# Performance work log

Measured on AMD Instinct MI355X. Metric: run time of the kernel, lower is better.

Reference implementation:

```python
import jax, jax.numpy as jnp
import numpy as np

# SmallViT config (reconstructed; see shape_source)
B, C, H, W = 1024, 3, 32, 32
P = 4                # patch size
D = 128              # embed dim
NH, DH = 4, 32       # heads, head dim
FF = 256             # mlp hidden
L = 4                # encoder layers
T = (H // P) * (W // P) + 1  # 65 tokens
NQ = 4               # qubits
EPS = 1e-5


def layer_norm(x, s, b):
    m = x.mean(-1, keepdims=True)
    v = ((x - m) ** 2).mean(-1, keepdims=True)
    return (x - m) * jax.lax.rsqrt(v + EPS) * s + b


def setup_inputs() -> dict:
    key = jax.random.key(0)
    ks = iter(jax.random.split(key, 32))
    w = lambda *shape: jax.random.normal(next(ks), shape, jnp.float32) * 0.02
    inp = {
        'x': jax.random.normal(next(ks), (B, C, H, W), jnp.float32),
        'patch_w': w(D, C, P, P),
        'patch_b': jnp.zeros((D,), jnp.float32),
        'cls_token': w(1, 1, D),
        'pos_embed': w(1, T, D),
        # stacked per-layer encoder params (torch Linear convention: [out,in])
        'qkv_w': w(L, 3 * D, D), 'qkv_b': jnp.zeros((L, 3 * D), jnp.float32),
        'out_w': w(L, D, D),     'out_b': jnp.zeros((L, D), jnp.float32),
        'ln1_s': jnp.ones((L, D), jnp.float32), 'ln1_b': jnp.zeros((L, D), jnp.float32),
        'ln2_s': jnp.ones((L, D), jnp.float32), 'ln2_b': jnp.zeros((L, D), jnp.float32),
        'ff1_w': w(L, FF, D), 'ff1_b': jnp.zeros((L, FF), jnp.float32),
        'ff2_w': w(L, D, FF), 'ff2_b': jnp.zeros((L, D), jnp.float32),
        # quantum_reduce: Linear(128,32) -> ReLU -> Linear(32,4)
        'qr1_w': w(32, D), 'qr1_b': jnp.zeros((32,), jnp.float32),
        'qr2_w': w(NQ, 32), 'qr2_b': jnp.zeros((NQ,), jnp.float32),
        'q_weights': jax.random.normal(next(ks), (NQ,), jnp.float32),
        'clf_w': w(10, D + NQ), 'clf_b': jnp.zeros((10,), jnp.float32),
    }
    return inp


def reference(x, patch_w, patch_b, cls_token, pos_embed,
              qkv_w, qkv_b, out_w, out_b, ln1_s, ln1_b, ln2_s, ln2_b,
              ff1_w, ff1_b, ff2_w, ff2_b,
              qr1_w, qr1_b, qr2_w, qr2_b, q_weights, clf_w, clf_b):
    b = x.shape[0]
    # patch embed: conv stride==kernel -> reshape + einsum
    xp = x.reshape(b, C, H // P, P, W // P, P)
    tok = jnp.einsum('bcipjq,dcpq->bijd', xp, patch_w).reshape(b, -1, D) + patch_b
    # prepend cls, add pos
    h = jnp.concatenate([jnp.broadcast_to(cls_token, (b, 1, D)), tok], axis=1) + pos_embed
    scale = 1.0 / np.sqrt(DH)
    for i in range(L):
        # self-attention (post-LN encoder layer)
        qkv = h @ qkv_w[i].T + qkv_b[i]                      # [b,T,3D]
        q, k, v = jnp.split(qkv, 3, axis=-1)
        q = q.reshape(b, T, NH, DH).transpose(0, 2, 1, 3)
        k = k.reshape(b, T, NH, DH).transpose(0, 2, 1, 3)
        v = v.reshape(b, T, NH, DH).transpose(0, 2, 1, 3)
        attn = jax.nn.softmax(jnp.einsum('bhqd,bhkd->bhqk', q, k) * scale, axis=-1)
        o = jnp.einsum('bhqk,bhkd->bhqd', attn, v).transpose(0, 2, 1, 3).reshape(b, T, D)
        o = o @ out_w[i].T + out_b[i]
        h = layer_norm(h + o, ln1_s[i], ln1_b[i])
        ff = jax.nn.relu(h @ ff1_w[i].T + ff1_b[i]) @ ff2_w[i].T + ff2_b[i]
        h = layer_norm(h + ff, ln2_s[i], ln2_b[i])
    cls_out = h[:, 0]                                         # [b,D]
    q_in = jnp.tanh(jax.nn.relu(cls_out @ qr1_w.T + qr1_b) @ qr2_w.T + qr2_b)  # [b,4]
    # closed-form 4-qubit circuit: RY(in) RX(w) + CNOT chain -> <Z_i> = cumprod cos(in)cos(w)
    q_out = jnp.cumprod(jnp.cos(q_in) * jnp.cos(q_weights)[None, :], axis=-1)
    combined = jnp.concatenate([cls_out, q_out], axis=1)      # [b,132]
    return combined @ clf_w.T + clf_b                         # [b,10]
```

## Files before the change

kernel.cpp:

```cpp
#include <hip/hip_runtime.h>

typedef unsigned short ushort_t;
typedef unsigned int   uint32;
typedef short s16x8 __attribute__((ext_vector_type(8)));
typedef float f32x4 __attribute__((ext_vector_type(4)));

#define HS    136
#define KOF   0
#define VOF   10880
#define PWOF  23168
#define BIGN  29312
#define EPS_  1e-5f
#define SCALE2_ 0.25503483f

#define MFMA16(a,b,c) __builtin_amdgcn_mfma_f32_16x16x32_bf16((a),(b),(c),0,0,0)

__device__ __forceinline__ float bfu(ushort_t u) {
  union { uint32 i; float f; } c; c.i = ((uint32)u) << 16; return c.f;
}
__device__ __forceinline__ void bf2(uint32 u, float& a, float& b) {
  union { uint32 i; float f; } c0, c1;
  c0.i = u << 16; c1.i = u & 0xffff0000u; a = c0.f; b = c1.f;
}
__device__ __forceinline__ ushort_t f2bf(float f) {
  union { float f; uint32 i; } c; c.f = f;
  uint32 r = c.i + 0x7fffu + ((c.i >> 16) & 1u);
  return (ushort_t)(r >> 16);
}

__device__ bool sniff_f32(const ushort_t* x) {
  int insane = 0, zeros = 0;
  for (int i = 0; i < 256; ++i) {
    ushort_t u = x[i];
    int e = (u >> 7) & 0xFF;
    if (u == 0) zeros++;
    else if (e == 0xFF || e < 0x60) insane++;
  }
  return (insane >= 16) || (zeros >= 64);
}

struct WPack {
  const void* src[23];
  unsigned    off[23];
  unsigned    n[23];
};

__global__ __launch_bounds__(256) void canon(WPack p, const ushort_t* x, ushort_t* dst,
                                             int* flagOut) {
  const bool f32 = sniff_f32(x);
  const int gid = blockIdx.x * blockDim.x + threadIdx.x;
  const int gsz = gridDim.x * blockDim.x;
  for (int a = 0; a < 23; ++a) {
    unsigned n = p.n[a];
    ushort_t* d = dst + p.off[a];
    if (f32) {
      const float* s = (const float*)p.src[a];
      for (unsigned i = gid; i < n; i += gsz) d[i] = f2bf(s[i]);
    } else {
      const ushort_t* s = (const ushort_t*)p.src[a];
      for (unsigned i = gid; i < n; i += gsz) d[i] = s[i];
    }
  }
  if (blockIdx.x == 0 && threadIdx.x == 0) *flagOut = f32 ? 1 : 0;
}

__global__ __launch_bounds__(256, 2)
void vit_fused(const ushort_t* __restrict__ x,
               const ushort_t* __restrict__ patch_w,
               const ushort_t* __restrict__ patch_b,
               const ushort_t* __restrict__ cls_token,
               const ushort_t* __restrict__ pos_embed,
               const ushort_t* __restrict__ qkv_w,
               const ushort_t* __restrict__ qkv_b,
               const ushort_t* __restrict__ out_w,
               const ushort_t* __restrict__ out_b,
               const ushort_t* __restrict__ ln1_s,
               const ushort_t* __restrict__ ln1_b,
               const ushort_t* __restrict__ ln2_s,
               const ushort_t* __restrict__ ln2_b,
               const ushort_t* __restrict__ ff1_w,
               const ushort_t* __restrict__ ff1_b,
               const ushort_t* __restrict__ ff2_w,
               const ushort_t* __restrict__ ff2_b,
               const ushort_t* __restrict__ qr1_w,
               const ushort_t* __restrict__ qr1_b,
               const ushort_t* __restrict__ qr2_w,
               const ushort_t* __restrict__ qr2_b,
               const ushort_t* __restrict__ q_weights,
               const ushort_t* __restrict__ clf_w,
               const ushort_t* __restrict__ clf_b,
               const int* __restrict__ flag,
               void* __restrict__ out)
{
  __shared__ __align__(16) ushort_t h_s[80 * HS];
  __shared__ __align__(16) ushort_t big[BIGN];

  const int tid  = threadIdx.x;
  const int wid  = tid >> 6;
  const int lane = tid & 63;
  const int lr   = lane & 15;
  const int lq   = lane >> 4;
  const int b    = blockIdx.x;
  const bool f32m = (*flag != 0);

  uint32* bx = (uint32*)big;
  if (f32m) {
    const float* xf = (const float*)x + (size_t)b * 3072;
    for (int i = tid; i < 1536; i += 256) {
      uint32 lo = f2bf(xf[2 * i]);
      uint32 hi = f2bf(xf[2 * i + 1]);
      bx[i] = lo | (hi << 16);
    }
  } else {
    const uint32* xb = (const uint32*)x + (size_t)b * 1536;
    for (int i = tid; i < 1536; i += 256) bx[i] = xb[i];
  }
  {
    const uint32* pw = (const uint32*)patch_w;
    for (int i = tid; i < 3072; i += 256) bx[1536 + i] = pw[i];
  }
  __syncthreads();

  #pragma unroll 1
  for (int it = 0; it < 32; ++it) {
    int idx = tid + 256 * it;
    int p = idx >> 7, d = idx & 127;
    int pi = p >> 3, pj = p & 7;
    float acc = 0.f;
    #pragma unroll
    for (int c = 0; c < 3; ++c) {
      #pragma unroll
      for (int py = 0; py < 4; ++py) {
        const uint32* xr = bx + ((c * 1024 + (pi * 4 + py) * 32 + pj * 4) >> 1);
        const uint32* wr = bx + 1536 + ((d * 48 + c * 16 + py * 4) >> 1);
        #pragma unroll
        for (int q2 = 0; q2 < 2; ++q2) {
          float xa, xb2, wa, wb;
          bf2(xr[q2], xa, xb2); bf2(wr[q2], wa, wb);
          acc += xa * wa + xb2 * wb;
        }
      }
    }
    acc += bfu(patch_b[d]) + bfu(pos_embed[(1 + p) * 128 + d]);
    h_s[(1 + p) * HS + d] = f2bf(acc);
  }
  if (tid < 128) h_s[tid] = f2bf(bfu(cls_token[tid]) + bfu(pos_embed[tid]));
  for (int i = tid; i < 15 * HS; i += 256) h_s[65 * HS + i] = 0;

  #pragma unroll 1
  for (int il = 0; il < 4; ++il) {
    __syncthreads();

    for (int i = tid; i < 2048; i += 256)
      big[VOF + (i >> 4) * 96 + 80 + (i & 15)] = 0;

    const ushort_t* Wqkv = qkv_w + (size_t)il * 384 * 128;
    const ushort_t* Bqkv = qkv_b + il * 384;
    const ushort_t* Wo   = out_w + (size_t)il * 128 * 128;
    ushort_t* bw = big + PWOF + wid * 1536;

    #pragma unroll 2
    for (int u = wid * 20; u < wid * 20 + 20; ++u) {
      int ty = u & 1, r = u >> 1;
      int mt = r >> 3, nt = r & 7;
      int m0 = mt * 16;
      int rb = (ty ? 256 : 128) + nt * 16;
      float bv = bfu(Bqkv[rb + lr]);
      f32x4 acc = {bv, bv, bv, bv};
      #pragma unroll
      for (int kc = 0; kc < 4; ++kc) {
        s16x8 a  = *(const s16x8*)&h_s[(m0 + lr) * HS + kc * 32 + lq * 8];
        s16x8 bb = *(const s16x8*)&Wqkv[(rb + lr) * 128 + kc * 32 + lq * 8];
        acc = MFMA16(a, bb, acc);
      }
      if (!ty) {
        #pragma unroll
        for (int i = 0; i < 4; ++i)
          big[KOF + (m0 + lq * 4 + i) * 136 + nt * 16 + lr] = f2bf(acc[i]);
      } else {
        uint32 w0 = (uint32)f2bf(acc[0]) | ((uint32)f2bf(acc[1]) << 16);
        uint32 w1 = (uint32)f2bf(acc[2]) | ((uint32)f2bf(acc[3]) << 16);
        uint32* dst = (uint32*)&big[VOF + (nt * 16 + lr) * 96 + m0 + lq * 4];
        dst[0] = w0; dst[1] = w1;
      }
    }
    __syncthreads();

    auto attn_one = [&](int m0) {
      s16x8 ha[4];
      #pragma unroll
      for (int kc = 0; kc < 4; ++kc)
        ha[kc] = *(const s16x8*)&h_s[(m0 + lr) * HS + kc * 32 + lq * 8];
      f32x4 opA[8];
      #pragma unroll
      for (int nt = 0; nt < 8; ++nt) {
        float bv = bfu(out_b[il * 128 + nt * 16 + lr]);
        opA[nt] = (f32x4){bv, bv, bv, bv};
      }
      #pragma unroll 1
      for (int ih = 0; ih < 4; ++ih) {
        #pragma unroll
        for (int n2 = 0; n2 < 2; ++n2) {
          int rb = ih * 32 + n2 * 16;
          float bv = bfu(Bqkv[rb + lr]);
          f32x4 acc = {bv, bv, bv, bv};
          #pragma unroll
          for (int kc = 0; kc < 4; ++kc) {
            s16x8 bb = *(const s16x8*)&Wqkv[(rb + lr) * 128 + kc * 32 + lq * 8];
            acc = MFMA16(ha[kc], bb, acc);
          }
          #pragma unroll
          for (int i = 0; i < 4; ++i)
            bw[(lq * 4 + i) * 40 + n2 * 16 + lr] = f2bf(acc[i] * SCALE2_);
        }
        s16x8 aq = *(const s16x8*)&bw[lr * 40 + lq * 8];
        f32x4 S[5];
        #pragma unroll
        for (int jt = 0; jt < 5; ++jt) {
          s16x8 bb = *(const s16x8*)&big[KOF + (jt * 16 + lr) * 136 + ih * 32 + lq * 8];
          f32x4 z = {0.f, 0.f, 0.f, 0.f};
          S[jt] = MFMA16(aq, bb, z);
        }
        float mx[4] = {-1e30f, -1e30f, -1e30f, -1e30f};
        #pragma unroll
        for (int jt = 0; jt < 5; ++jt)
          #pragma unroll
          for (int i = 0; i < 4; ++i) {
            float sv = S[jt][i];
            if (jt == 4 && lr > 0) sv = -1e30f;
            S[jt][i] = sv;
            mx[i] = fmaxf(mx[i], sv);
          }
        #pragma unroll
        for (int off = 1; off < 16; off <<= 1)
          #pragma unroll
          for (int i = 0; i < 4; ++i) mx[i] = fmaxf(mx[i], __shfl_xor(mx[i], off));
        float sm[4] = {0.f, 0.f, 0.f, 0.f};
        #pragma unroll
        for (int jt = 0; jt < 5; ++jt)
          #pragma unroll
          for (int i = 0; i < 4; ++i) {
            float pv = exp2f(S[jt][i] - mx[i]);
            S[jt][i] = pv; sm[i] += pv;
          }
        #pragma unroll
        for (int off = 1; off < 16; off <<= 1)
          #pragma unroll
          for (int i = 0; i < 4; ++i) sm[i] += __shfl_xor(sm[i], off);
        float inv[4];
        #pragma unroll
        for (int i = 0; i < 4; ++i) inv[i] = 1.f / sm[i];
        #pragma unroll
        for (int i = 0; i < 4; ++i) {
          #pragma unroll
          for (int jt = 0; jt < 5; ++jt)
            bw[(lq * 4 + i) * 96 + jt * 16 + lr] = f2bf(S[jt][i] * inv[i]);
          bw[(lq * 4 + i) * 96 + 80 + lr] = 0;
        }
        f32x4 ov[2];
        #pragma unroll
        for (int n2 = 0; n2 < 2; ++n2) {
          f32x4 acc = {0.f, 0.f, 0.f, 0.f};
          #pragma unroll
          for (int kc = 0; kc < 3; ++kc) {
            s16x8 a  = *(const s16x8*)&bw[lr * 96 + kc * 32 + lq * 8];
            s16x8 bb = *(const s16x8*)&big[VOF + (ih * 32 + n2 * 16 + lr) * 96 + kc * 32 + lq * 8];
            acc = MFMA16(a, bb, acc);
          }
          ov[n2] = acc;
        }
        #pragma unroll
        for (int n2 = 0; n2 < 2; ++n2)
          #pragma unroll
          for (int i = 0; i < 4; ++i)
            bw[(lq * 4 + i) * 40 + n2 * 16 + lr] = f2bf(ov[n2][i]);
        s16x8 ao = *(const s16x8*)&bw[lr * 40 + lq * 8];
        #pragma unroll
        for (int nt = 0; nt < 8; ++nt) {
          s16x8 bb = *(const s16x8*)&Wo[(nt * 16 + lr) * 128 + ih * 32 + lq * 8];
          opA[nt] = MFMA16(ao, bb, opA[nt]);
        }
      }

      float sv[4] = {0, 0, 0, 0}, ssv[4] = {0, 0, 0, 0};
      #pragma unroll
      for (int nt = 0; nt < 8; ++nt)
        #pragma unroll
        for (int i = 0; i < 4; ++i) {
          float r = opA[nt][i] + bfu(h_s[(m0 + lq * 4 + i) * HS + nt * 16 + lr]);
          opA[nt][i] = r; sv[i] += r; ssv[i] += r * r;
        }
      #pragma unroll
      for (int off = 1; off < 16; off <<= 1)
        #pragma unroll
        for (int i = 0; i < 4; ++i) {
          sv[i]  += __shfl_xor(sv[i], off);
          ssv[i] += __shfl_xor(ssv[i], off);
        }
      float mean[4], inv2[4];
      #pragma unroll
      for (int i = 0; i < 4; ++i) {
        mean[i] = sv[i] * (1.f / 128.f);
        inv2[i] = rsqrtf(fmaxf(ssv[i] * (1.f / 128.f) - mean[i] * mean[i], 0.f) + EPS_);
      }
      #pragma unroll
      for (int nt = 0; nt < 8; ++nt) {
        float g  = bfu(ln1_s[il * 128 + nt * 16 + lr]);
        float be = bfu(ln1_b[il * 128 + nt * 16 + lr]);
        #pragma unroll
        for (int i = 0; i < 4; ++i)
          h_s[(m0 + lq * 4 + i) * HS + nt * 16 + lr] =
              f2bf((opA[nt][i] - mean[i]) * inv2[i] * g + be);
      }
    };
    attn_one(wid * 16);
    if (wid == 3) attn_one(64);
    __syncthreads();

    {
      const ushort_t* W1 = ff1_w + (size_t)il * 256 * 128;
      const ushort_t* W2 = ff2_w + (size_t)il * 128 * 256;
      ushort_t* fsl = big + KOF + wid * 2176;
      int nFF = (wid == 0) ? 2 : 1;
      #pragma unroll 1
      for (int s = 0; s < nFF; ++s) {
        int mt = (s == 0) ? wid : 4;
        int m0 = mt * 16;
        s16x8 ha[4];
        #pragma unroll
        for (int kc = 0; kc < 4; ++kc)
          ha[kc] = *(const s16x8*)&h_s[(m0 + lr) * HS + kc * 32 + lq * 8];
        f32x4 acc2[8];
        #pragma unroll
        for (int nt = 0; nt < 8; ++nt) {
          float bv = bfu(ff2_b[il * 128 + nt * 16 + lr]);
          acc2[nt] = (f32x4){bv, bv, bv, bv};
        }
        #pragma unroll 1
        for (int half = 0; half < 2; ++half) {
          #pragma unroll 1
          for (int n8 = 0; n8 < 8; ++n8) {
            int ng = half * 8 + n8;
            float bv = bfu(ff1_b[il * 256 + ng * 16 + lr]);
            f32x4 acc = {bv, bv, bv, bv};
            #pragma unroll
            for (int kc = 0; kc < 4; ++kc) {
              s16x8 bb = *(const s16x8*)&W1[(ng * 16 + lr) * 128 + kc * 32 + lq * 8];
              acc = MFMA16(ha[kc], bb, acc);
            }
            #pragma unroll
            for (int i = 0; i < 4; ++i)
              fsl[(lq * 4 + i) * 136 + n8 * 16 + lr] = f2bf(fmaxf(acc[i], 0.f));
          }
          #pragma unroll
          for (int kc = 0; kc < 4; ++kc) {
            s16x8 a2 = *(const s16x8*)&fsl[lr * 136 + kc * 32 + lq * 8];
            #pragma unroll
            for (int nt = 0; nt < 8; ++nt) {
              s16x8 bb = *(const s16x8*)&W2[(nt * 16 + lr) * 256 + half * 128 + kc * 32 + lq * 8];
              acc2[nt] = MFMA16(a2, bb, acc2[nt]);
            }
          }
        }
        float sv[4] = {0, 0, 0, 0}, ssv[4] = {0, 0, 0, 0};
        #pragma unroll
        for (int nt = 0; nt < 8; ++nt)
          #pragma unroll
          for (int i = 0; i < 4; ++i) {
            float r = acc2[nt][i] + bfu(h_s[(m0 + lq * 4 + i) * HS + nt * 16 + lr]);
            acc2[nt][i] = r; sv[i] += r; ssv[i] += r * r;
          }
        #pragma unroll
        for (int off = 1; off < 16; off <<= 1)
          #pragma unroll
          for (int i = 0; i < 4; ++i) {
            sv[i]  += __shfl_xor(sv[i], off);
            ssv[i] += __shfl_xor(ssv[i], off);
          }
        float mean[4], inv2[4];
        #pragma unroll
        for (int i = 0; i < 4; ++i) {
          mean[i] = sv[i] * (1.f / 128.f);
          inv2[i] = rsqrtf(fmaxf(ssv[i] * (1.f / 128.f) - mean[i] * mean[i], 0.f) + EPS_);
        }
        #pragma unroll
        for (int nt = 0; nt < 8; ++nt) {
          float g  = bfu(ln2_s[il * 128 + nt * 16 + lr]);
          float be = bfu(ln2_b[il * 128 + nt * 16 + lr]);
          #pragma unroll
          for (int i = 0; i < 4; ++i)
            h_s[(m0 + lq * 4 + i) * HS + nt * 16 + lr] =
                f2bf((acc2[nt][i] - mean[i]) * inv2[i] * g + be);
        }
      }
    }
  }

  __syncthreads();
  float* scr = (float*)big;
  {
    int j = tid & 31;
    const uint32* hrow0 = (const uint32*)h_s;
    const uint32* w = (const uint32*)qr1_w + j * 64;
    float acc = 0.f;
    #pragma unroll 4
    for (int k2 = 0; k2 < 64; ++k2) {
      float ha, hb, wa, wb;
      bf2(hrow0[k2], ha, hb); bf2(w[k2], wa, wb);
      acc += ha * wa + hb * wb;
    }
    float u = fmaxf(acc + bfu(qr1_b[j]), 0.f);
    if (tid < 32) scr[tid] = u;
  }
  __syncthreads();
  if (tid < 10) {
    float qo[4]; float cp = 1.f;
    #pragma unroll
    for (int j2 = 0; j2 < 4; ++j2) {
      float acc = 0.f;
      #pragma unroll
      for (int k = 0; k < 32; ++k) acc += scr[k] * bfu(qr2_w[j2 * 32 + k]);
      float qin = tanhf(acc + bfu(qr2_b[j2]));
      cp *= cosf(qin) * cosf(bfu(q_weights[j2]));
      qo[j2] = cp;
    }
    const uint32* hrow0 = (const uint32*)h_s;
    const uint32* cw = (const uint32*)clf_w + tid * 66;
    float acc = 0.f;
    #pragma unroll 4
    for (int k2 = 0; k2 < 64; ++k2) {
      float ha, hb, wa, wb;
      bf2(hrow0[k2], ha, hb); bf2(cw[k2], wa, wb);
      acc += ha * wa + hb * wb;
    }
    #pragma unroll
    for (int d = 0; d < 4; ++d) acc += qo[d] * bfu(clf_w[tid * 132 + 128 + d]);
    acc += bfu(clf_b[tid]);
    if (f32m) ((float*)out)[b * 10 + tid] = acc;
    else      ((ushort_t*)out)[b * 10 + tid] = f2bf(acc);
  }
}

extern "C" void kernel_launch(void* const* d_in, const int* in_sizes, int n_in,
                              void* d_out, int out_size, void* d_ws, size_t ws_size,
                              hipStream_t stream) {
  WPack p;
  unsigned cur = 0;
  for (int i = 0; i < 23; ++i) {
    p.src[i] = d_in[i + 1];
    p.off[i] = cur;
    p.n[i]   = (unsigned)in_sizes[i + 1];
    cur += (p.n[i] + 7u) & ~7u;
  }
  ushort_t* wsb = (ushort_t*)d_ws;
  unsigned flag_off = (cur * 2 + 3u) & ~3u;
  int* flagp = (int*)((char*)d_ws + flag_off);
  const ushort_t* x = (const ushort_t*)d_in[0];

  canon<<<dim3(128), dim3(256), 0, stream>>>(p, x, wsb, flagp);

  int B = out_size / 10;
  vit_fused<<<dim3(B), dim3(256), 0, stream>>>(
      x,
      wsb + p.off[0],  wsb + p.off[1],  wsb + p.off[2],  wsb + p.off[3],
      wsb + p.off[4],  wsb + p.off[5],  wsb + p.off[6],  wsb + p.off[7],
      wsb + p.off[8],  wsb + p.off[9],  wsb + p.off[10], wsb + p.off[11],
      wsb + p.off[12], wsb + p.off[13], wsb + p.off[14], wsb + p.off[15],
      wsb + p.off[16], wsb + p.off[17], wsb + p.off[18], wsb + p.off[19],
      wsb + p.off[20], wsb + p.off[21], wsb + p.off[22],
      flagp, d_out);
}
```

Baseline: 901.1 us.

## Use five waves per block so each wave owns one token tile end-to-end

The block grows from four to five wavefronts, so each wave owns one 16-row token tile. The old scheme gave wave 3 a second attention tile and wave 0 a second FFN tile. Attention and FFN are fused into one per-wave pass, which removes the barrier between them. The V/probability layout is shrunk from 96 to 72 columns, and the 65th key is handled with a scalar shuffle-multiply instead of a third MFMA chunk. The aim is to remove the load imbalance and the extra sync, at the cost of more threads and registers per block and a reshuffled shared-memory layout.

After: 874.5 us. 1.03x faster.

```diff
diff --git a/kernel.cpp b/kernel.cpp
--- a/kernel.cpp
+++ b/kernel.cpp
@@ -7,9 +7,9 @@
 
 #define HS    136
 #define KOF   0
-#define VOF   10880
-#define PWOF  23168
-#define BIGN  29312
+#define VOF   9248
+#define SLOF  18464
+#define BIGN  29344
 #define EPS_  1e-5f
 #define SCALE2_ 0.25503483f
 
@@ -64,7 +64,7 @@
   if (blockIdx.x == 0 && threadIdx.x == 0) *flagOut = f32 ? 1 : 0;
 }
 
-__global__ __launch_bounds__(256, 2)
+__global__ __launch_bounds__(320, 2)
 void vit_fused(const ushort_t* __restrict__ x,
                const ushort_t* __restrict__ patch_w,
                const ushort_t* __restrict__ patch_b,
@@ -102,28 +102,28 @@
   const int lq   = lane >> 4;
   const int b    = blockIdx.x;
   const bool f32m = (*flag != 0);
+  const int m0 = wid * 16;
 
   uint32* bx = (uint32*)big;
   if (f32m) {
     const float* xf = (const float*)x + (size_t)b * 3072;
-    for (int i = tid; i < 1536; i += 256) {
+    for (int i = tid; i < 1536; i += 320) {
       uint32 lo = f2bf(xf[2 * i]);
       uint32 hi = f2bf(xf[2 * i + 1]);
       bx[i] = lo | (hi << 16);
     }
   } else {
     const uint32* xb = (const uint32*)x + (size_t)b * 1536;
-    for (int i = tid; i < 1536; i += 256) bx[i] = xb[i];
+    for (int i = tid; i < 1536; i += 320) bx[i] = xb[i];
   }
   {
     const uint32* pw = (const uint32*)patch_w;
-    for (int i = tid; i < 3072; i += 256) bx[1536 + i] = pw[i];
+    for (int i = tid; i < 3072; i += 320) bx[1536 + i] = pw[i];
   }
   __syncthreads();
 
   #pragma unroll 1
-  for (int it = 0; it < 32; ++it) {
-    int idx = tid + 256 * it;
+  for (int idx = tid; idx < 8192; idx += 320) {
     int p = idx >> 7, d = idx & 127;
     int pi = p >> 3, pj = p & 7;
     float acc = 0.f;
@@ -145,48 +145,50 @@
     h_s[(1 + p) * HS + d] = f2bf(acc);
   }
   if (tid < 128) h_s[tid] = f2bf(bfu(cls_token[tid]) + bfu(pos_embed[tid]));
-  for (int i = tid; i < 15 * HS; i += 256) h_s[65 * HS + i] = 0;
+  for (int i = tid; i < 15 * HS; i += 320) h_s[65 * HS + i] = 0;
 
   #pragma unroll 1
   for (int il = 0; il < 4; ++il) {
     __syncthreads();
 
-    for (int i = tid; i < 2048; i += 256)
-      big[VOF + (i >> 4) * 96 + 80 + (i & 15)] = 0;
-
     const ushort_t* Wqkv = qkv_w + (size_t)il * 384 * 128;
     const ushort_t* Bqkv = qkv_b + il * 384;
     const ushort_t* Wo   = out_w + (size_t)il * 128 * 128;
-    ushort_t* bw = big + PWOF + wid * 1536;
+    ushort_t* bw = big + SLOF + wid * 2176;
 
     #pragma unroll 2
-    for (int u = wid * 20; u < wid * 20 + 20; ++u) {
+    for (int u = wid * 16; u < wid * 16 + 16; ++u) {
       int ty = u & 1, r = u >> 1;
       int mt = r >> 3, nt = r & 7;
-      int m0 = mt * 16;
+      int km0 = mt * 16;
       int rb = (ty ? 256 : 128) + nt * 16;
       float bv = bfu(Bqkv[rb + lr]);
       f32x4 acc = {bv, bv, bv, bv};
       #pragma unroll
       for (int kc = 0; kc < 4; ++kc) {
-        s16x8 a  = *(const s16x8*)&h_s[(m0 + lr) * HS + kc * 32 + lq * 8];
+        s16x8 a  = *(const s16x8*)&h_s[(km0 + lr) * HS + kc * 32 + lq * 8];
         s16x8 bb = *(const s16x8*)&Wqkv[(rb + lr) * 128 + kc * 32 + lq * 8];
         acc = MFMA16(a, bb, acc);
       }
       if (!ty) {
         #pragma unroll
-        for (int i = 0; i < 4; ++i)
-          big[KOF + (m0 + lq * 4 + i) * 136 + nt * 16 + lr] = f2bf(acc[i]);
+        for (int i = 0; i < 4; ++i) {
+          int row = km0 + lq * 4 + i;
+          if (row < 68) big[KOF + row * 136 + nt * 16 + lr] = f2bf(acc[i]);
+        }
       } else {
-        uint32 w0 = (uint32)f2bf(acc[0]) | ((uint32)f2bf(acc[1]) << 16);
-        uint32 w1 = (uint32)f2bf(acc[2]) | ((uint32)f2bf(acc[3]) << 16);
-        uint32* dst = (uint32*)&big[VOF + (nt * 16 + lr) * 96 + m0 + lq * 4];
-        dst[0] = w0; dst[1] = w1;
+        int tk = km0 + lq * 4;
+        if (tk < 68) {
+          uint32 w0 = (uint32)f2bf(acc[0]) | ((uint32)f2bf(acc[1]) << 16);
+          uint32 w1 = (uint32)f2bf(acc[2]) | ((uint32)f2bf(acc[3]) << 16);
+          uint32* dst = (uint32*)&big[VOF + (nt * 16 + lr) * 72 + tk];
+          dst[0] = w0; dst[1] = w1;
+        }
       }
     }
     __syncthreads();
 
-    auto attn_one = [&](int m0) {
+    {
       s16x8 ha[4];
       #pragma unroll
       for (int kc = 0; kc < 4; ++kc)
@@ -251,21 +253,25 @@
         #pragma unroll
         for (int i = 0; i < 4; ++i) inv[i] = 1.f / sm[i];
         #pragma unroll
-        for (int i = 0; i < 4; ++i) {
-          #pragma unroll
-          for (int jt = 0; jt < 5; ++jt)
-            bw[(lq * 4 + i) * 96 + jt * 16 + lr] = f2bf(S[jt][i] * inv[i]);
-          bw[(lq * 4 + i) * 96 + 80 + lr] = 0;
-        }
+        for (int i = 0; i < 4; ++i)
+          #pragma unroll
+          for (int jt = 0; jt < 4; ++jt)
+            bw[(lq * 4 + i) * 72 + jt * 16 + lr] = f2bf(S[jt][i] * inv[i]);
         f32x4 ov[2];
         #pragma unroll
         for (int n2 = 0; n2 < 2; ++n2) {
           f32x4 acc = {0.f, 0.f, 0.f, 0.f};
           #pragma unroll
-          for (int kc = 0; kc < 3; ++kc) {
-            s16x8 a  = *(const s16x8*)&bw[lr * 96 + kc * 32 + lq * 8];
-            s16x8 bb = *(const s16x8*)&big[VOF + (ih * 32 + n2 * 16 + lr) * 96 + kc * 32 + lq * 8];
+          for (int kc = 0; kc < 2; ++kc) {
+            s16x8 a  = *(const s16x8*)&bw[lr * 72 + kc * 32 + lq * 8];
+            s16x8 bb = *(const s16x8*)&big[VOF + (ih * 32 + n2 * 16 + lr) * 72 + kc * 32 + lq * 8];
             acc = MFMA16(a, bb, acc);
+          }
+          float v64 = bfu(big[VOF + (ih * 32 + n2 * 16 + lr) * 72 + 64]);
+          #pragma unroll
+          for (int i = 0; i < 4; ++i) {
+            float p64 = __shfl(S[4][i], lane & 48) * inv[i];
+            acc[i] += p64 * v64;
           }
           ov[n2] = acc;
         }
@@ -312,86 +318,74 @@
           h_s[(m0 + lq * 4 + i) * HS + nt * 16 + lr] =
               f2bf((opA[nt][i] - mean[i]) * inv2[i] * g + be);
       }
-    };
-    attn_one(wid * 16);
-    if (wid == 3) attn_one(64);
-    __syncthreads();
-
-    {
+
       const ushort_t* W1 = ff1_w + (size_t)il * 256 * 128;
       const ushort_t* W2 = ff2_w + (size_t)il * 128 * 256;
-      ushort_t* fsl = big + KOF + wid * 2176;
-      int nFF = (wid == 0) ? 2 : 1;
+      s16x8 hf[4];
+      #pragma unroll
+      for (int kc = 0; kc < 4; ++kc)
+        hf[kc] = *(const s16x8*)&h_s[(m0 + lr) * HS + kc * 32 + lq * 8];
+      f32x4 acc2[8];
+      #pragma unroll
+      for (int nt = 0; nt < 8; ++nt) {
+        float bv = bfu(ff2_b[il * 128 + nt * 16 + lr]);
+        acc2[nt] = (f32x4){bv, bv, bv, bv};
+      }
       #pragma unroll 1
-      for (int s = 0; s < nFF; ++s) {
-        int mt = (s == 0) ? wid : 4;
-        int m0 = mt * 16;
-        s16x8 ha[4];
-        #pragma unroll
-        for (int kc = 0; kc < 4; ++kc)
-          ha[kc] = *(const s16x8*)&h_s[(m0 + lr) * HS + kc * 32 + lq * 8];
-        f32x4 acc2[8];
-        #pragma unroll
-        for (int nt = 0; nt < 8; ++nt) {
-          float bv = bfu(ff2_b[il * 128 + nt * 16 + lr]);
-          acc2[nt] = (f32x4){bv, bv, bv, bv};
-        }
-        #pragma unroll 1
-        for (int half = 0; half < 2; ++half) {
-          #pragma unroll 1
-          for (int n8 = 0; n8 < 8; ++n8) {
-            int ng = half * 8 + n8;
-            float bv = bfu(ff1_b[il * 256 + ng * 16 + lr]);
-            f32x4 acc = {bv, bv, bv, bv};
-            #pragma unroll
-            for (int kc = 0; kc < 4; ++kc) {
-              s16x8 bb = *(const s16x8*)&W1[(ng * 16 + lr) * 128 + kc * 32 + lq * 8];
-              acc = MFMA16(ha[kc], bb, acc);
-            }
-            #pragma unroll
-            for (int i = 0; i < 4; ++i)
-              fsl[(lq * 4 + i) * 136 + n8 * 16 + lr] = f2bf(fmaxf(acc[i], 0.f));
-          }
+      for (int half = 0; half < 2; ++half) {
+        #pragma unroll 2
+        for (int n8 = 0; n8 < 8; ++n8) {
+          int ng = half * 8 + n8;
+          float bv = bfu(ff1_b[il * 256 + ng * 16 + lr]);
+          f32x4 acc = {bv, bv, bv, bv};
           #pragma unroll
           for (int kc = 0; kc < 4; ++kc) {
-            s16x8 a2 = *(const s16x8*)&fsl[lr * 136 + kc * 32 + lq * 8];
-            #pragma unroll
-            for (int nt = 0; nt < 8; ++nt) {
-              s16x8 bb = *(const s16x8*)&W2[(nt * 16 + lr) * 256 + half * 128 + kc * 32 + lq * 8];
-              acc2[nt] = MFMA16(a2, bb, acc2[nt]);
-            }
-          }
-        }
-        float sv[4] = {0, 0, 0, 0}, ssv[4] = {0, 0, 0, 0};
-        #pragma unroll
-        for (int nt = 0; nt < 8; ++nt)
-          #pragma unroll
-          for (int i = 0; i < 4; ++i) {
-            float r = acc2[nt][i] + bfu(h_s[(m0 + lq * 4 + i) * HS + nt * 16 + lr]);
-            acc2[nt][i] = r; sv[i] += r; ssv[i] += r * r;
-          }
-        #pragma unroll
-        for (int off = 1; off < 16; off <<= 1)
-          #pragma unroll
-          for (int i = 0; i < 4; ++i) {
-            sv[i]  += __shfl_xor(sv[i], off);
-            ssv[i] += __shfl_xor(ssv[i], off);
-          }
-        float mean[4], inv2[4];
+            s16x8 bb = *(const s16x8*)&W1[(ng * 16 + lr) * 128 + kc * 32 + lq * 8];
+            acc = MFMA16(hf[kc], bb, acc);
+          }
+          #pragma unroll
+          for (int i = 0; i < 4; ++i)
+            bw[(lq * 4 + i) * 136 + n8 * 16 + lr] = f2bf(fmaxf(acc[i], 0.f));
+        }
+        #pragma unroll
+        for (int kc = 0; kc < 4; ++kc) {
+          s16x8 a2 = *(const s16x8*)&bw[lr * 136 + kc * 32 + lq * 8];
+          #pragma unroll
+          for (int nt = 0; nt < 8; ++nt) {
+            s16x8 bb = *(const s16x8*)&W2[(nt * 16 + lr) * 256 + half * 128 + kc * 32 + lq * 8];
+            acc2[nt] = MFMA16(a2, bb, acc2[nt]);
+          }
+        }
+      }
+      float s2[4] = {0, 0, 0, 0}, ss2[4] = {0, 0, 0, 0};
+      #pragma unroll
+      for (int nt = 0; nt < 8; ++nt)
         #pragma unroll
         for (int i = 0; i < 4; ++i) {
-          mean[i] = sv[i] * (1.f / 128.f);
-          inv2[i] = rsqrtf(fmaxf(ssv[i] * (1.f / 128.f) - mean[i] * mean[i], 0.f) + EPS_);
-        }
-        #pragma unroll
-        for (int nt = 0; nt < 8; ++nt) {
-          float g  = bfu(ln2_s[il * 128 + nt * 16 + lr]);
-          float be = bfu(ln2_b[il * 128 + nt * 16 + lr]);
-          #pragma unroll
-          for (int i = 0; i < 4; ++i)
-            h_s[(m0 + lq * 4 + i) * HS + nt * 16 + lr] =
-                f2bf((acc2[nt][i] - mean[i]) * inv2[i] * g + be);
-        }
+          float r = acc2[nt][i] + bfu(h_s[(m0 + lq * 4 + i) * HS + nt * 16 + lr]);
+          acc2[nt][i] = r; s2[i] += r; ss2[i] += r * r;
+        }
+      #pragma unroll
+      for (int off = 1; off < 16; off <<= 1)
+        #pragma unroll
+        for (int i = 0; i < 4; ++i) {
+          s2[i]  += __shfl_xor(s2[i], off);
+          ss2[i] += __shfl_xor(ss2[i], off);
+        }
+      float mean2[4], invb[4];
+      #pragma unroll
+      for (int i = 0; i < 4; ++i) {
+        mean2[i] = s2[i] * (1.f / 128.f);
+        invb[i]  = rsqrtf(fmaxf(ss2[i] * (1.f / 128.f) - mean2[i] * mean2[i], 0.f) + EPS_);
+      }
+      #pragma unroll
+      for (int nt = 0; nt < 8; ++nt) {
+        float g  = bfu(ln2_s[il * 128 + nt * 16 + lr]);
+        float be = bfu(ln2_b[il * 128 + nt * 16 + lr]);
+        #pragma unroll
+        for (int i = 0; i < 4; ++i)
+          h_s[(m0 + lq * 4 + i) * HS + nt * 16 + lr] =
+              f2bf((acc2[nt][i] - mean2[i]) * invb[i] * g + be);
       }
     }
   }
@@ -460,7 +454,7 @@
   canon<<<dim3(128), dim3(256), 0, stream>>>(p, x, wsb, flagp);
 
   int B = out_size / 10;
-  vit_fused<<<dim3(B), dim3(256), 0, stream>>>(
+  vit_fused<<<dim3(B), dim3(320), 0, stream>>>(
       x,
       wsb + p.off[0],  wsb + p.off[1],  wsb + p.off[2],  wsb + p.off[3],
       wsb + p.off[4],  wsb + p.off[5],  wsb + p.off[6],  wsb + p.off[7],
```
